# Optimization experiments

Hardware: AMD Instinct MI355X
Metric: run time of the kernel (lower is better)

## Reference

```python
import jax, jax.numpy as jnp
import numpy as np

HEIGHT, WIDTH, NUM_FRAMES, DIM = 64, 64, 16, 1280
GRIDS = [(8, 32, 32), (16, 16, 16), (4, 48, 48), (1, 64, 64)]  # ragged (t,h,w) per sample


def _sincos_1d(embed_dim, t_size):
    # matches get_1d_sincos_pos_embed_from_grid
    omega = np.arange(embed_dim // 2, dtype=np.float32) / (embed_dim / 2.0)
    omega = 1.0 / (10000.0 ** omega)
    pos = np.arange(t_size, dtype=np.float32)
    out = np.einsum('m,d->md', pos, omega)
    return np.concatenate([np.sin(out), np.cos(out)], axis=1).astype(np.float32)  # [t, dim]


def setup_inputs() -> dict:
    key = jax.random.key(0)
    k1, k2 = jax.random.split(key)
    total_tokens = sum(t * h * w for t, h, w in GRIDS)  # 25600
    x = jax.random.normal(k1, (total_tokens, DIM), dtype=jnp.float32)
    weight = jax.random.normal(k2, (HEIGHT, WIDTH, DIM), dtype=jnp.float32)  # learnable 2D pos emb
    time_weight = jnp.asarray(_sincos_1d(DIM, NUM_FRAMES))  # [num_frames, dim] sincos buffer
    grid_thws = np.asarray(GRIDS, dtype=np.int64)  # static per-sample (t,h,w)
    return {"x": x, "weight": weight, "time_weight": time_weight, "grid_thws": grid_thws}


def reference(x, weight, time_weight, grid_thws):
    H, W, D = weight.shape
    grids = np.asarray(grid_thws).tolist()  # static metadata; loop is over ragged samples
    pos_embs = []
    for t, h, w in grids:
        if (h, w) == (H, W):
            pe2d = weight.reshape(-1, D)  # [h*w, D]
        else:
            # torch path: fp32 bicubic interpolation of [H,W,D] -> [h,w,D]
            pe2d = jax.image.resize(weight.astype(jnp.float32), (h, w, D),
                                    method='bicubic').astype(x.dtype).reshape(-1, D)
        if t == 1:
            pe3d = pe2d
        else:
            # broadcast-add temporal sincos embedding: [t,1,D] + [1,h*w,D]
            pe3d = (pe2d[None, :, :] + time_weight[:t, None, :]).reshape(-1, D)
        pos_embs.append(pe3d)
    return x + jnp.concatenate(pos_embs, axis=0)
```

## Files before the change

kernel.cpp:

```cpp
#include <hip/hip_runtime.h>


#define PE32_OFF 0
#define PE16_OFF 1310720
#define PE48_OFF 1638400

__device__ __forceinline__ float keys_cubic(float x) {
    x = fabsf(x);
    if (x >= 2.0f) return 0.0f;
    if (x >= 1.0f) return ((-0.5f * x + 2.5f) * x - 4.0f) * x + 2.0f;
    return ((1.5f * x - 2.5f) * x) * x + 1.0f;
}

__device__ __forceinline__ void tap_params(int o, int out_size,
                                           int& i0, int& n, float& sf,
                                           float& inv_ks, float& inv_sum) {
    float inv_scale = 64.0f / (float)out_size;
    float ks = inv_scale;
    float radius = 2.0f * ks;
    sf = ((float)o + 0.5f) * inv_scale - 0.5f;
    int lo = (int)ceilf(sf - radius); if (lo < 0) lo = 0;
    int hi = (int)floorf(sf + radius); if (hi > 63) hi = 63;
    n = hi - lo + 1;
    i0 = lo;
    inv_ks = 1.0f / ks;
    float sum = 0.0f;
    for (int k = 0; k < n; ++k)
        sum += keys_cubic((sf - (float)(lo + k)) * inv_ks);
    inv_sum = 1.0f / sum;
}

#define TMP_STRIDE 68
__global__ __launch_bounds__(256) void resize2d_kernel(const float* __restrict__ weight,
                                                       float* __restrict__ ws) {
    int td  = blockIdx.x % 20;
    int row = blockIdx.x / 20;
    int out_h, out_w, oy; float* pe_base;
    if (row < 32)      { out_h = 32; out_w = 32; oy = row;      pe_base = ws + PE32_OFF; }
    else if (row < 48) { out_h = 16; out_w = 16; oy = row - 32; pe_base = ws + PE16_OFF; }
    else               { out_h = 48; out_w = 48; oy = row - 48; pe_base = ws + PE48_OFF; }
    int d0 = td * 64;

    __shared__ float tmp[64 * TMP_STRIDE];

    int i0, nh; float sfh, ikh, ish;
    tap_params(oy, out_h, i0, nh, sfh, ikh, ish);

    for (int item = threadIdx.x; item < 1024; item += 256) {
        int x  = item >> 4;
        int f4 = item & 15;
        const float* src = weight + (size_t)x * 1280 + d0 + (f4 << 2);
        float4 acc = make_float4(0.f, 0.f, 0.f, 0.f);
        for (int k = 0; k < nh; ++k) {
            float c = keys_cubic((sfh - (float)(i0 + k)) * ikh);
            float4 v = *(const float4*)(src + (size_t)(i0 + k) * (64 * 1280));
            acc.x += c * v.x; acc.y += c * v.y; acc.z += c * v.z; acc.w += c * v.w;
        }
        acc.x *= ish; acc.y *= ish; acc.z *= ish; acc.w *= ish;
        *(float4*)&tmp[x * TMP_STRIDE + (f4 << 2)] = acc;
    }
    __syncthreads();

    int nitems = out_w << 4;
    for (int item = threadIdx.x; item < nitems; item += 256) {
        int ox = item >> 4;
        int f4 = item & 15;
        int j0, nw; float sfw, ikw, isw;
        tap_params(ox, out_w, j0, nw, sfw, ikw, isw);
        float4 acc = make_float4(0.f, 0.f, 0.f, 0.f);
        for (int k = 0; k < nw; ++k) {
            float c = keys_cubic((sfw - (float)(j0 + k)) * ikw);
            float4 v = *(const float4*)&tmp[(j0 + k) * TMP_STRIDE + (f4 << 2)];
            acc.x += c * v.x; acc.y += c * v.y; acc.z += c * v.z; acc.w += c * v.w;
        }
        acc.x *= isw; acc.y *= isw; acc.z *= isw; acc.w *= isw;
        *(float4*)(pe_base + (size_t)(oy * out_w + ox) * 1280 + d0 + (f4 << 2)) = acc;
    }
}

__global__ __launch_bounds__(256) void add_pe_kernel(const float* __restrict__ x,
                                                     const float* __restrict__ weight,
                                                     const float* __restrict__ tw,
                                                     const float* __restrict__ ws,
                                                     float* __restrict__ out) {
    int v = blockIdx.x * 256 + threadIdx.x;
    int token = v / 320;
    int d = (v - token * 320) << 2;

    const float* pe;
    int frame;
    if (token < 8192) {
        frame = token >> 10;
        int px = token & 1023;
        pe = ws + PE32_OFF + (size_t)px * 1280;
    } else if (token < 12288) {
        int l = token - 8192;
        frame = l >> 8;
        int px = l & 255;
        pe = ws + PE16_OFF + (size_t)px * 1280;
    } else if (token < 21504) {
        int l = token - 12288;
        frame = l / 2304;
        int px = l - frame * 2304;
        pe = ws + PE48_OFF + (size_t)px * 1280;
    } else {
        int l = token - 21504;
        frame = -1;
        pe = weight + (size_t)l * 1280;
    }

    size_t off = (size_t)token * 1280 + d;
    float4 xv = *(const float4*)(x + off);
    float4 pv = *(const float4*)(pe + d);
    float4 o = make_float4(xv.x + pv.x, xv.y + pv.y, xv.z + pv.z, xv.w + pv.w);
    if (frame >= 0) {
        float4 tv = *(const float4*)(tw + (size_t)frame * 1280 + d);
        o.x += tv.x; o.y += tv.y; o.z += tv.z; o.w += tv.w;
    }
    *(float4*)(out + off) = o;
}

extern "C" void kernel_launch(void* const* d_in, const int* in_sizes, int n_in,
                              void* d_out, int out_size, void* d_ws, size_t ws_size,
                              hipStream_t stream) {
    const float* x      = (const float*)d_in[0];
    const float* weight = (const float*)d_in[1];
    const float* tw     = (const float*)d_in[2];
    float* ws  = (float*)d_ws;
    float* out = (float*)d_out;

    hipLaunchKernelGGL(resize2d_kernel, dim3(1920), dim3(256), 0, stream, weight, ws);
    hipLaunchKernelGGL(add_pe_kernel, dim3(32000), dim3(256), 0, stream, x, weight, tw, ws, out);
}
```

Measured before the change: 266.5 us.

## Fuse bicubic resize with positional-embedding add, keeping PE rows in registers

Merges the resize kernel and the add kernel into one launch. Each block computes one interpolated PE row slice into registers, then loops over all frames, adding x, PE and the temporal embedding and writing the output directly. Extra blocks handle the full-resolution sample. This removes the workspace write and reread of the PE tables and one kernel launch. In exchange, parallelism per block becomes serial over frames, and the grid is smaller with uneven work per block (t ranges from 4 to 16).

Measured after the change: 276.2 us. 3.7% more time.

```diff
diff --git a/kernel.cpp b/kernel.cpp
--- a/kernel.cpp
+++ b/kernel.cpp
@@ -1,9 +1,5 @@
 #include <hip/hip_runtime.h>
 
-
-#define PE32_OFF 0
-#define PE16_OFF 1310720
-#define PE48_OFF 1638400
 
 __device__ __forceinline__ float keys_cubic(float x) {
     x = fabsf(x);
@@ -31,93 +27,101 @@
 }
 
 #define TMP_STRIDE 68
-__global__ __launch_bounds__(256) void resize2d_kernel(const float* __restrict__ weight,
-                                                       float* __restrict__ ws) {
-    int td  = blockIdx.x % 20;
-    int row = blockIdx.x / 20;
-    int out_h, out_w, oy; float* pe_base;
-    if (row < 32)      { out_h = 32; out_w = 32; oy = row;      pe_base = ws + PE32_OFF; }
-    else if (row < 48) { out_h = 16; out_w = 16; oy = row - 32; pe_base = ws + PE16_OFF; }
-    else               { out_h = 48; out_w = 48; oy = row - 48; pe_base = ws + PE48_OFF; }
+
+__global__ __launch_bounds__(256) void fused_pe_kernel(const float* __restrict__ x,
+                                                       const float* __restrict__ weight,
+                                                       const float* __restrict__ tw,
+                                                       float* __restrict__ out) {
+    int td     = blockIdx.x % 20;
+    int row_id = blockIdx.x / 20;
     int d0 = td * 64;
+
+    if (row_id >= 96) {
+        int y = row_id - 96;
+        #pragma unroll
+        for (int k = 0; k < 4; ++k) {
+            int item = threadIdx.x + (k << 8);
+            int px = item >> 4;
+            int f4 = item & 15;
+            size_t woff = (size_t)(y * 64 + px) * 1280 + d0 + (f4 << 2);
+            size_t off  = (size_t)(21504 + y * 64 + px) * 1280 + d0 + (f4 << 2);
+            float4 wv = *(const float4*)(weight + woff);
+            float4 xv = *(const float4*)(x + off);
+            float4 o  = make_float4(xv.x + wv.x, xv.y + wv.y, xv.z + wv.z, xv.w + wv.w);
+            *(float4*)(out + off) = o;
+        }
+        return;
+    }
+
+    int out_h, out_w, oy, t, tok_base;
+    if (row_id < 32)      { out_h = 32; out_w = 32; oy = row_id;      t = 8;  tok_base = 0; }
+    else if (row_id < 48) { out_h = 16; out_w = 16; oy = row_id - 32; t = 16; tok_base = 8192; }
+    else                  { out_h = 48; out_w = 48; oy = row_id - 48; t = 4;  tok_base = 12288; }
+    int npx = out_h * out_w;
 
     __shared__ float tmp[64 * TMP_STRIDE];
 
     int i0, nh; float sfh, ikh, ish;
     tap_params(oy, out_h, i0, nh, sfh, ikh, ish);
 
-    for (int item = threadIdx.x; item < 1024; item += 256) {
-        int x  = item >> 4;
+    #pragma unroll
+    for (int k = 0; k < 4; ++k) {
+        int item = threadIdx.x + (k << 8);
+        int xc = item >> 4;
         int f4 = item & 15;
-        const float* src = weight + (size_t)x * 1280 + d0 + (f4 << 2);
+        const float* src = weight + (size_t)xc * 1280 + d0 + (f4 << 2);
         float4 acc = make_float4(0.f, 0.f, 0.f, 0.f);
-        for (int k = 0; k < nh; ++k) {
-            float c = keys_cubic((sfh - (float)(i0 + k)) * ikh);
-            float4 v = *(const float4*)(src + (size_t)(i0 + k) * (64 * 1280));
+        for (int j = 0; j < nh; ++j) {
+            float c = keys_cubic((sfh - (float)(i0 + j)) * ikh);
+            float4 v = *(const float4*)(src + (size_t)(i0 + j) * (64 * 1280));
             acc.x += c * v.x; acc.y += c * v.y; acc.z += c * v.z; acc.w += c * v.w;
         }
         acc.x *= ish; acc.y *= ish; acc.z *= ish; acc.w *= ish;
-        *(float4*)&tmp[x * TMP_STRIDE + (f4 << 2)] = acc;
+        *(float4*)&tmp[xc * TMP_STRIDE + (f4 << 2)] = acc;
     }
     __syncthreads();
 
     int nitems = out_w << 4;
-    for (int item = threadIdx.x; item < nitems; item += 256) {
-        int ox = item >> 4;
-        int f4 = item & 15;
-        int j0, nw; float sfw, ikw, isw;
-        tap_params(ox, out_w, j0, nw, sfw, ikw, isw);
-        float4 acc = make_float4(0.f, 0.f, 0.f, 0.f);
-        for (int k = 0; k < nw; ++k) {
-            float c = keys_cubic((sfw - (float)(j0 + k)) * ikw);
-            float4 v = *(const float4*)&tmp[(j0 + k) * TMP_STRIDE + (f4 << 2)];
-            acc.x += c * v.x; acc.y += c * v.y; acc.z += c * v.z; acc.w += c * v.w;
+    float4 pe_reg[3];
+    #pragma unroll
+    for (int k = 0; k < 3; ++k) {
+        int item = threadIdx.x + (k << 8);
+        if (item < nitems) {
+            int ox = item >> 4;
+            int f4 = item & 15;
+            int j0, nw; float sfw, ikw, isw;
+            tap_params(ox, out_w, j0, nw, sfw, ikw, isw);
+            float4 acc = make_float4(0.f, 0.f, 0.f, 0.f);
+            for (int j = 0; j < nw; ++j) {
+                float c = keys_cubic((sfw - (float)(j0 + j)) * ikw);
+                float4 v = *(const float4*)&tmp[(j0 + j) * TMP_STRIDE + (f4 << 2)];
+                acc.x += c * v.x; acc.y += c * v.y; acc.z += c * v.z; acc.w += c * v.w;
+            }
+            acc.x *= isw; acc.y *= isw; acc.z *= isw; acc.w *= isw;
+            pe_reg[k] = acc;
         }
-        acc.x *= isw; acc.y *= isw; acc.z *= isw; acc.w *= isw;
-        *(float4*)(pe_base + (size_t)(oy * out_w + ox) * 1280 + d0 + (f4 << 2)) = acc;
-    }
-}
-
-__global__ __launch_bounds__(256) void add_pe_kernel(const float* __restrict__ x,
-                                                     const float* __restrict__ weight,
-                                                     const float* __restrict__ tw,
-                                                     const float* __restrict__ ws,
-                                                     float* __restrict__ out) {
-    int v = blockIdx.x * 256 + threadIdx.x;
-    int token = v / 320;
-    int d = (v - token * 320) << 2;
-
-    const float* pe;
-    int frame;
-    if (token < 8192) {
-        frame = token >> 10;
-        int px = token & 1023;
-        pe = ws + PE32_OFF + (size_t)px * 1280;
-    } else if (token < 12288) {
-        int l = token - 8192;
-        frame = l >> 8;
-        int px = l & 255;
-        pe = ws + PE16_OFF + (size_t)px * 1280;
-    } else if (token < 21504) {
-        int l = token - 12288;
-        frame = l / 2304;
-        int px = l - frame * 2304;
-        pe = ws + PE48_OFF + (size_t)px * 1280;
-    } else {
-        int l = token - 21504;
-        frame = -1;
-        pe = weight + (size_t)l * 1280;
     }
 
-    size_t off = (size_t)token * 1280 + d;
-    float4 xv = *(const float4*)(x + off);
-    float4 pv = *(const float4*)(pe + d);
-    float4 o = make_float4(xv.x + pv.x, xv.y + pv.y, xv.z + pv.z, xv.w + pv.w);
-    if (frame >= 0) {
-        float4 tv = *(const float4*)(tw + (size_t)frame * 1280 + d);
-        o.x += tv.x; o.y += tv.y; o.z += tv.z; o.w += tv.w;
+    for (int f = 0; f < t; ++f) {
+        int frame_tok = tok_base + f * npx + oy * out_w;
+        const float* twf = tw + (size_t)f * 1280 + d0;
+        #pragma unroll
+        for (int k = 0; k < 3; ++k) {
+            int item = threadIdx.x + (k << 8);
+            if (item < nitems) {
+                int ox = item >> 4;
+                int f4 = item & 15;
+                float4 tv = *(const float4*)(twf + (f4 << 2));
+                size_t off = (size_t)(frame_tok + ox) * 1280 + d0 + (f4 << 2);
+                float4 xv = *(const float4*)(x + off);
+                float4 o = make_float4(xv.x + pe_reg[k].x + tv.x,
+                                       xv.y + pe_reg[k].y + tv.y,
+                                       xv.z + pe_reg[k].z + tv.z,
+                                       xv.w + pe_reg[k].w + tv.w);
+                *(float4*)(out + off) = o;
+            }
+        }
     }
-    *(float4*)(out + off) = o;
 }
 
 extern "C" void kernel_launch(void* const* d_in, const int* in_sizes, int n_in,
@@ -126,9 +130,8 @@
     const float* x      = (const float*)d_in[0];
     const float* weight = (const float*)d_in[1];
     const float* tw     = (const float*)d_in[2];
-    float* ws  = (float*)d_ws;
     float* out = (float*)d_out;
 
-    hipLaunchKernelGGL(resize2d_kernel, dim3(1920), dim3(256), 0, stream, weight, ws);
-    hipLaunchKernelGGL(add_pe_kernel, dim3(32000), dim3(256), 0, stream, x, weight, tw, ws, out);
+    hipLaunchKernelGGL(fused_pe_kernel, dim3(3200), dim3(256), 0, stream,
+                       x, weight, tw, out);
 }
```

## Move full-size sample add into resize kernel and batch loads in add kernel

Applied to the files above, without the earlier changes.

The untouched 64x64 sample (x + weight) is now processed by extra blocks appended to the resize kernel, so its traffic overlaps with the resize work. The add kernel then covers only the three temporal samples, with each thread handling four float4 items whose loads are all issued before any compute, which raises memory-level parallelism and cuts the block count. The per-token frame branch is gone. The cost is higher register pressure and a longer-running first kernel.

Result: slower. 273.5 us (+2.6%).

```diff
diff --git a/kernel.cpp b/kernel.cpp
--- a/kernel.cpp
+++ b/kernel.cpp
@@ -31,33 +31,64 @@
 }
 
 #define TMP_STRIDE 68
-__global__ __launch_bounds__(256) void resize2d_kernel(const float* __restrict__ weight,
-                                                       float* __restrict__ ws) {
+
+__global__ __launch_bounds__(256) void resize_and_s3_kernel(const float* __restrict__ x,
+                                                            const float* __restrict__ weight,
+                                                            float* __restrict__ ws,
+                                                            float* __restrict__ out) {
+    if (blockIdx.x >= 1920) {
+        int b = blockIdx.x - 1920;
+        int td = b % 20;
+        int y  = b / 20;
+        int d0 = td * 64;
+        size_t woff[4], off[4];
+        float4 wv[4], xv[4];
+        #pragma unroll
+        for (int k = 0; k < 4; ++k) {
+            int item = threadIdx.x + (k << 8);
+            int px = item >> 4;
+            int f4 = item & 15;
+            woff[k] = (size_t)(y * 64 + px) * 1280 + d0 + (f4 << 2);
+            off[k]  = (size_t)(21504 + y * 64 + px) * 1280 + d0 + (f4 << 2);
+            wv[k] = *(const float4*)(weight + woff[k]);
+            xv[k] = *(const float4*)(x + off[k]);
+        }
+        #pragma unroll
+        for (int k = 0; k < 4; ++k) {
+            float4 o = make_float4(xv[k].x + wv[k].x, xv[k].y + wv[k].y,
+                                   xv[k].z + wv[k].z, xv[k].w + wv[k].w);
+            *(float4*)(out + off[k]) = o;
+        }
+        return;
+    }
+
     int td  = blockIdx.x % 20;
     int row = blockIdx.x / 20;
+    int d0 = td * 64;
     int out_h, out_w, oy; float* pe_base;
     if (row < 32)      { out_h = 32; out_w = 32; oy = row;      pe_base = ws + PE32_OFF; }
     else if (row < 48) { out_h = 16; out_w = 16; oy = row - 32; pe_base = ws + PE16_OFF; }
     else               { out_h = 48; out_w = 48; oy = row - 48; pe_base = ws + PE48_OFF; }
-    int d0 = td * 64;
 
     __shared__ float tmp[64 * TMP_STRIDE];
 
     int i0, nh; float sfh, ikh, ish;
     tap_params(oy, out_h, i0, nh, sfh, ikh, ish);
 
-    for (int item = threadIdx.x; item < 1024; item += 256) {
-        int x  = item >> 4;
+    #pragma unroll
+    for (int k = 0; k < 4; ++k) {
+        int item = threadIdx.x + (k << 8);
+        int xc = item >> 4;
         int f4 = item & 15;
-        const float* src = weight + (size_t)x * 1280 + d0 + (f4 << 2);
+        const float* src = weight + (size_t)xc * 1280 + d0 + (f4 << 2);
         float4 acc = make_float4(0.f, 0.f, 0.f, 0.f);
-        for (int k = 0; k < nh; ++k) {
-            float c = keys_cubic((sfh - (float)(i0 + k)) * ikh);
-            float4 v = *(const float4*)(src + (size_t)(i0 + k) * (64 * 1280));
+        for (int j = 0; j < nh; ++j) {
+            float c = keys_cubic((sfh - (float)(i0 + j)) * ikh);
+            float4 v = *(const float4*)(src + (size_t)(i0 + j) * (64 * 1280));
             acc.x += c * v.x; acc.y += c * v.y; acc.z += c * v.z; acc.w += c * v.w;
         }
         acc.x *= ish; acc.y *= ish; acc.z *= ish; acc.w *= ish;
-        *(float4*)&tmp[x * TMP_STRIDE + (f4 << 2)] = acc;
+        *(float4*)&tmp[xc * TMP_STRIDE + (f4 << 2)] = acc;
     }
     __syncthreads();
 
@@ -68,9 +99,9 @@
         int j0, nw; float sfw, ikw, isw;
         tap_params(ox, out_w, j0, nw, sfw, ikw, isw);
         float4 acc = make_float4(0.f, 0.f, 0.f, 0.f);
-        for (int k = 0; k < nw; ++k) {
-            float c = keys_cubic((sfw - (float)(j0 + k)) * ikw);
-            float4 v = *(const float4*)&tmp[(j0 + k) * TMP_STRIDE + (f4 << 2)];
+        for (int j = 0; j < nw; ++j) {
+            float c = keys_cubic((sfw - (float)(j0 + j)) * ikw);
+            float4 v = *(const float4*)&tmp[(j0 + j) * TMP_STRIDE + (f4 << 2)];
             acc.x += c * v.x; acc.y += c * v.y; acc.z += c * v.z; acc.w += c * v.w;
         }
         acc.x *= isw; acc.y *= isw; acc.z *= isw; acc.w *= isw;
@@ -79,45 +110,45 @@
 }
 
 __global__ __launch_bounds__(256) void add_pe_kernel(const float* __restrict__ x,
-                                                     const float* __restrict__ weight,
                                                      const float* __restrict__ tw,
                                                      const float* __restrict__ ws,
                                                      float* __restrict__ out) {
+    const int G = 6720 * 256;
     int v = blockIdx.x * 256 + threadIdx.x;
-    int token = v / 320;
-    int d = (v - token * 320) << 2;
 
-    const float* pe;
-    int frame;
-    if (token < 8192) {
-        frame = token >> 10;
-        int px = token & 1023;
-        pe = ws + PE32_OFF + (size_t)px * 1280;
-    } else if (token < 12288) {
-        int l = token - 8192;
-        frame = l >> 8;
-        int px = l & 255;
-        pe = ws + PE16_OFF + (size_t)px * 1280;
-    } else if (token < 21504) {
-        int l = token - 12288;
-        frame = l / 2304;
-        int px = l - frame * 2304;
-        pe = ws + PE48_OFF + (size_t)px * 1280;
-    } else {
-        int l = token - 21504;
-        frame = -1;
-        pe = weight + (size_t)l * 1280;
+    size_t off[4];
+    float4 xv[4], pv[4], tv[4];
+    #pragma unroll
+    for (int b = 0; b < 4; ++b) {
+        int item = v + b * G;
+        int token = item / 320;
+        int d = (item - token * 320) << 2;
+        const float* pe; int frame;
+        if (token < 8192) {
+            frame = token >> 10;
+            pe = ws + PE32_OFF + (size_t)(token & 1023) * 1280;
+        } else if (token < 12288) {
+            int l = token - 8192;
+            frame = l >> 8;
+            pe = ws + PE16_OFF + (size_t)(l & 255) * 1280;
+        } else {
+            int l = token - 12288;
+            frame = l / 2304;
+            pe = ws + PE48_OFF + (size_t)(l - frame * 2304) * 1280;
+        }
+        off[b] = (size_t)token * 1280 + d;
+        xv[b] = *(const float4*)(x + off[b]);
+        pv[b] = *(const float4*)(pe + d);
+        tv[b] = *(const float4*)(tw + (size_t)frame * 1280 + d);
     }
-
-    size_t off = (size_t)token * 1280 + d;
-    float4 xv = *(const float4*)(x + off);
-    float4 pv = *(const float4*)(pe + d);
-    float4 o = make_float4(xv.x + pv.x, xv.y + pv.y, xv.z + pv.z, xv.w + pv.w);
-    if (frame >= 0) {
-        float4 tv = *(const float4*)(tw + (size_t)frame * 1280 + d);
-        o.x += tv.x; o.y += tv.y; o.z += tv.z; o.w += tv.w;
+    #pragma unroll
+    for (int b = 0; b < 4; ++b) {
+        float4 o = make_float4(xv[b].x + pv[b].x + tv[b].x,
+                               xv[b].y + pv[b].y + tv[b].y,
+                               xv[b].z + pv[b].z + tv[b].z,
+                               xv[b].w + pv[b].w + tv[b].w);
+        *(float4*)(out + off[b]) = o;
     }
-    *(float4*)(out + off) = o;
 }
 
 extern "C" void kernel_launch(void* const* d_in, const int* in_sizes, int n_in,
@@ -129,6 +160,8 @@
     float* ws  = (float*)d_ws;
     float* out = (float*)d_out;
 
-    hipLaunchKernelGGL(resize2d_kernel, dim3(1920), dim3(256), 0, stream, weight, ws);
-    hipLaunchKernelGGL(add_pe_kernel, dim3(32000), dim3(256), 0, stream, x, weight, tw, ws, out);
+    hipLaunchKernelGGL(resize_and_s3_kernel, dim3(3200), dim3(256), 0, stream,
+                       x, weight, ws, out);
+    hipLaunchKernelGGL(add_pe_kernel, dim3(6720), dim3(256), 0, stream,
+                       x, tw, ws, out);
 }
```
